# Performance work log

Hardware: AMD Instinct MI355X
Metric: run time of the kernel (lower is better)

## Reference

```python
import jax, jax.numpy as jnp
import numpy as np

HIDDEN = 1024

def setup_inputs() -> dict:
    key = jax.random.key(0)
    ks = jax.random.split(key, 7)
    s = 1.0 / np.sqrt(HIDDEN)
    X = jax.random.normal(ks[0], (4, 2048, HIDDEN), dtype=jnp.float32)
    Wq = jax.random.uniform(ks[1], (HIDDEN, HIDDEN), jnp.float32, -s, s)
    bq = jax.random.uniform(ks[2], (HIDDEN,), jnp.float32, -s, s)
    Wk = jax.random.uniform(ks[3], (HIDDEN, HIDDEN), jnp.float32, -s, s)
    bk = jax.random.uniform(ks[4], (HIDDEN,), jnp.float32, -s, s)
    Wv = jax.random.uniform(ks[5], (HIDDEN, HIDDEN), jnp.float32, -s, s)
    bv = jax.random.uniform(ks[6], (HIDDEN,), jnp.float32, -s, s)
    return {"X": X, "Wq": Wq, "bq": bq, "Wk": Wk, "bk": bk, "Wv": Wv, "bv": bv}

def reference(X, Wq, bq, Wk, bk, Wv, bv):
    # torch Linear: x @ W.T + b
    q = jnp.einsum('bsd,ed->bse', X, Wq) + bq  # [B,S,H]
    k = jnp.einsum('bsd,ed->bse', X, Wk) + bk
    v = jnp.einsum('bsd,ed->bse', X, Wv) + bv
    scores = jnp.einsum('bqd,bkd->bqk', q, k) / jnp.sqrt(jnp.float32(HIDDEN))  # [B,S,S]
    attn = jax.nn.softmax(scores, axis=-1)
    return jnp.einsum('bqk,bkd->bqd', attn, v)
```

## Files before the change

### kernel.cpp

```cpp
#include <hip/hip_runtime.h>
#include <hip/hip_bf16.h>
#include <stdint.h>

#define B_ 4
#define S_ 2048
#define H_ 1024

typedef __attribute__((ext_vector_type(4))) float f32x4;
typedef __attribute__((ext_vector_type(8))) short bf16x8;

#define AS1C(p) ((const __attribute__((address_space(1))) void*)(p))
#define AS3(p)  ((__attribute__((address_space(3))) void*)(p))

__global__ __launch_bounds__(256)
void f32_to_bf16_k(const float* __restrict__ in, __hip_bfloat16* __restrict__ out, int n4) {
    int i = blockIdx.x * blockDim.x + threadIdx.x;
    if (i < n4) {
        float4 v = ((const float4*)in)[i];
        union { __hip_bfloat16 h[4]; uint64_t u; } o;
        o.h[0] = __float2bfloat16(v.x);
        o.h[1] = __float2bfloat16(v.y);
        o.h[2] = __float2bfloat16(v.z);
        o.h[3] = __float2bfloat16(v.w);
        ((uint64_t*)out)[i] = o.u;
    }
}

__global__ __launch_bounds__(256)
void pack_bias_k(const float* __restrict__ b0, const float* __restrict__ b1,
                 const float* __restrict__ b2, float* __restrict__ out) {
    int i = blockIdx.x * blockDim.x + threadIdx.x;
    const float* src = (i < H_) ? b0 : (i < 2 * H_) ? b1 : b2;
    out[i] = src[i & (H_ - 1)];
}

template<bool OUT_BF16, bool HAS_BIAS>
__global__ __launch_bounds__(256)
void gemm_bt(const __hip_bfloat16* __restrict__ A, int lda, long long aBatch,
             const __hip_bfloat16* __restrict__ B, int ldb, long long bBatch,
             const float* __restrict__ bias,
             void* __restrict__ Cout, int ldc, long long cBatch,
             int M, int N, int K, float scale)
{
    __shared__ __hip_bfloat16 lA[128 * 64];
    __shared__ __hip_bfloat16 lB[128 * 64];

    const int t  = threadIdx.x;
    const int bz = blockIdx.z;
    A += (long long)bz * aBatch;
    B += (long long)bz * bBatch;
    const int bm = blockIdx.y * 128;
    const int bn = blockIdx.x * 128;

    const int wave = t >> 6;
    const int lane = t & 63;
    const int wm = (wave & 1) * 64;
    const int wn = (wave >> 1) * 64;
    const int lm = lane & 15;
    const int kq = lane >> 4;

    f32x4 acc[4][4] = {};

    const int srow = t >> 3;
    const int swz  = ((t & 7) ^ ((t >> 3) & 7)) * 8;
    const __hip_bfloat16* gA = A + (long long)(bm + srow) * lda + swz;
    const __hip_bfloat16* gB = B + (long long)(bn + srow) * ldb + swz;
    __hip_bfloat16* sA = lA + t * 8;
    __hip_bfloat16* sB = lB + t * 8;

    const int cro = lm & 7;

    for (int k0 = 0; k0 < K; k0 += 64) {
        __syncthreads();
#pragma unroll
        for (int s = 0; s < 4; ++s) {
            __builtin_amdgcn_global_load_lds(AS1C(gA + (long long)s * 32 * lda + k0),
                                             AS3(sA + s * 2048), 16, 0, 0);
            __builtin_amdgcn_global_load_lds(AS1C(gB + (long long)s * 32 * ldb + k0),
                                             AS3(sB + s * 2048), 16, 0, 0);
        }
        __syncthreads();

#pragma unroll
        for (int ks = 0; ks < 2; ++ks) {
            bf16x8 af[4], bfr[4];
            const int ch = ((ks * 4 + kq) ^ cro) * 8;
#pragma unroll
            for (int i = 0; i < 4; ++i) {
                af[i]  = *(const bf16x8*)(lA + (wm + i * 16 + lm) * 64 + ch);
                bfr[i] = *(const bf16x8*)(lB + (wn + i * 16 + lm) * 64 + ch);
            }
#pragma unroll
            for (int i = 0; i < 4; ++i)
#pragma unroll
                for (int j = 0; j < 4; ++j)
                    acc[i][j] = __builtin_amdgcn_mfma_f32_16x16x32_bf16(af[i], bfr[j], acc[i][j], 0, 0, 0);
        }
    }

    const int r0 = kq * 4;
#pragma unroll
    for (int j = 0; j < 4; ++j) {
        const int col = bn + wn + j * 16 + lm;
        float bvv = 0.0f;
        if (HAS_BIAS) bvv = bias[col];
#pragma unroll
        for (int i = 0; i < 4; ++i) {
            const int rowb = bm + wm + i * 16 + r0;
#pragma unroll
            for (int r = 0; r < 4; ++r) {
                float val = acc[i][j][r] * scale + bvv;
                long long idx = (long long)bz * cBatch + (long long)(rowb + r) * ldc + col;
                if (OUT_BF16) ((__hip_bfloat16*)Cout)[idx] = __float2bfloat16(val);
                else          ((float*)Cout)[idx] = val;
            }
        }
    }
}

__global__ __launch_bounds__(256)
void transpose64(const __hip_bfloat16* __restrict__ in, int ld_in, long long inBatch,
                 __hip_bfloat16* __restrict__ out, long long outBatch,
                 int rows, int cols)
{
    __shared__ __hip_bfloat16 tile[64][66];
    in  += (long long)blockIdx.z * inBatch;
    out += (long long)blockIdx.z * outBatch;
    const int c0 = blockIdx.x * 64;
    const int r0 = blockIdx.y * 64;
    const int tc  = threadIdx.x & 63;
    const int tr4 = threadIdx.x >> 6;
#pragma unroll
    for (int r = tr4; r < 64; r += 4)
        tile[r][tc] = in[(long long)(r0 + r) * ld_in + c0 + tc];
    __syncthreads();
#pragma unroll
    for (int r = tr4; r < 64; r += 4)
        out[(long long)(c0 + r) * rows + r0 + tc] = tile[tc][r];
}

__global__ __launch_bounds__(256)
void softmax_rows(__hip_bfloat16* __restrict__ s, int cols)
{
    __shared__ float red[4];
    __shared__ float red2[4];
    __hip_bfloat16* p = s + (long long)blockIdx.x * cols;
    const int t = threadIdx.x;

    union { uint4 u; __hip_bfloat16 h[8]; } in;
    in.u = *(const uint4*)(p + t * 8);
    float v[8];
    float mx = -1e30f;
#pragma unroll
    for (int i = 0; i < 8; ++i) {
        v[i] = __bfloat162float(in.h[i]);
        mx = fmaxf(mx, v[i]);
    }
#pragma unroll
    for (int off = 32; off; off >>= 1) mx = fmaxf(mx, __shfl_down(mx, off));
    if ((t & 63) == 0) red[t >> 6] = mx;
    __syncthreads();
    mx = fmaxf(fmaxf(red[0], red[1]), fmaxf(red[2], red[3]));

    float sum = 0.0f;
#pragma unroll
    for (int i = 0; i < 8; ++i) { v[i] = __expf(v[i] - mx); sum += v[i]; }
#pragma unroll
    for (int off = 32; off; off >>= 1) sum += __shfl_down(sum, off);
    if ((t & 63) == 0) red2[t >> 6] = sum;
    __syncthreads();
    sum = red2[0] + red2[1] + red2[2] + red2[3];
    float inv = 1.0f / sum;
    union { uint4 u; __hip_bfloat16 h[8]; } o;
#pragma unroll
    for (int i = 0; i < 8; ++i) o.h[i] = __float2bfloat16(v[i] * inv);
    *(uint4*)(p + t * 8) = o.u;
}

extern "C" void kernel_launch(void* const* d_in, const int* in_sizes, int n_in,
                              void* d_out, int out_size, void* d_ws, size_t ws_size,
                              hipStream_t stream)
{
    const float* X  = (const float*)d_in[0];
    const float* Wq = (const float*)d_in[1];
    const float* bq = (const float*)d_in[2];
    const float* Wk = (const float*)d_in[3];
    const float* bk = (const float*)d_in[4];
    const float* Wv = (const float*)d_in[5];
    const float* bv = (const float*)d_in[6];
    float* out = (float*)d_out;

    char* w = (char*)d_ws;
    const size_t MB = 1ull << 20;
    __hip_bfloat16* Xb   = (__hip_bfloat16*)(w + 0);
    __hip_bfloat16* Wall = (__hip_bfloat16*)(w + 16 * MB);
    float*          ball = (float*)        (w + 22 * MB);
    __hip_bfloat16* sc   = (__hip_bfloat16*)(w + 0);
    __hip_bfloat16* qkv  = (__hip_bfloat16*)(w + 32 * MB);
    __hip_bfloat16* vtb  = (__hip_bfloat16*)(w + 80 * MB);

    const int HH4 = H_ * H_ / 4;

    f32_to_bf16_k<<<(B_ * S_ * H_ / 4 + 255) / 256, 256, 0, stream>>>(X, Xb, B_ * S_ * H_ / 4);
    f32_to_bf16_k<<<(HH4 + 255) / 256, 256, 0, stream>>>(Wq, Wall, HH4);
    f32_to_bf16_k<<<(HH4 + 255) / 256, 256, 0, stream>>>(Wk, Wall + H_ * H_, HH4);
    f32_to_bf16_k<<<(HH4 + 255) / 256, 256, 0, stream>>>(Wv, Wall + 2 * H_ * H_, HH4);
    pack_bias_k<<<(3 * H_) / 256, 256, 0, stream>>>(bq, bk, bv, ball);

    dim3 g1(3 * H_ / 128, (B_ * S_) / 128, 1);
    gemm_bt<true, true><<<g1, 256, 0, stream>>>(
        Xb, H_, 0, Wall, H_, 0, ball, qkv, 3 * H_, 0, B_ * S_, 3 * H_, H_, 1.0f);

    transpose64<<<dim3(H_ / 64, S_ / 64, B_), 256, 0, stream>>>(
        qkv + 2 * H_, 3 * H_, (long long)S_ * 3 * H_, vtb, (long long)H_ * S_, S_, H_);

    dim3 g2(S_ / 128, S_ / 128, B_);
    gemm_bt<true, false><<<g2, 256, 0, stream>>>(
        qkv,      3 * H_, (long long)S_ * 3 * H_,
        qkv + H_, 3 * H_, (long long)S_ * 3 * H_,
        nullptr, sc, S_, (long long)S_ * S_, S_, S_, H_, 0.03125f);

    softmax_rows<<<B_ * S_, 256, 0, stream>>>(sc, S_);

    dim3 g3(H_ / 128, S_ / 128, B_);
    gemm_bt<false, false><<<g3, 256, 0, stream>>>(
        sc,  S_, (long long)S_ * S_,
        vtb, S_, (long long)H_ * S_,
        nullptr, out, H_, (long long)S_ * H_, S_, H_, S_, 1.0f);
}
```

Before: 271.3 us.

## Switch GEMM to 32x32x16 MFMA, fuse V transpose into QKV epilogue, merge weight converts

Moves the GEMM inner loop from 16x16x32 to 32x32x16 bf16 MFMA with a 2x2 accumulator tile per wave, which cuts LDS fragment loads per MFMA. The QKV projection epilogue now writes the V block directly transposed into the vtb buffer, so the separate transpose kernel and its extra read and write pass go away. The three weight conversion launches are merged into one kernel. The transposed V stores are 8-byte column-strided writes, which may coalesce less well than the old row stores.

```diff
diff --git a/kernel.cpp b/kernel.cpp
--- a/kernel.cpp
+++ b/kernel.cpp
@@ -6,7 +6,7 @@
 #define S_ 2048
 #define H_ 1024
 
-typedef __attribute__((ext_vector_type(4))) float f32x4;
+typedef __attribute__((ext_vector_type(16))) float f32x16;
 typedef __attribute__((ext_vector_type(8))) short bf16x8;
 
 #define AS1C(p) ((const __attribute__((address_space(1))) void*)(p))
@@ -27,6 +27,22 @@
 }
 
 __global__ __launch_bounds__(256)
+void conv_weights_k(const float* __restrict__ w0, const float* __restrict__ w1,
+                    const float* __restrict__ w2, __hip_bfloat16* __restrict__ out) {
+    const int per = H_ * H_ / 4;
+    int i = blockIdx.x * blockDim.x + threadIdx.x;
+    const float* src = (i < per) ? w0 : (i < 2 * per) ? w1 : w2;
+    int li = i - ((i < per) ? 0 : (i < 2 * per) ? per : 2 * per);
+    float4 v = ((const float4*)src)[li];
+    union { __hip_bfloat16 h[4]; uint64_t u; } o;
+    o.h[0] = __float2bfloat16(v.x);
+    o.h[1] = __float2bfloat16(v.y);
+    o.h[2] = __float2bfloat16(v.z);
+    o.h[3] = __float2bfloat16(v.w);
+    ((uint64_t*)out)[i] = o.u;
+}
+
+__global__ __launch_bounds__(256)
 void pack_bias_k(const float* __restrict__ b0, const float* __restrict__ b1,
                  const float* __restrict__ b2, float* __restrict__ out) {
     int i = blockIdx.x * blockDim.x + threadIdx.x;
@@ -34,12 +50,13 @@
     out[i] = src[i & (H_ - 1)];
 }
 
-template<bool OUT_BF16, bool HAS_BIAS>
+template<bool OUT_BF16, bool HAS_BIAS, bool V_SPLIT>
 __global__ __launch_bounds__(256)
 void gemm_bt(const __hip_bfloat16* __restrict__ A, int lda, long long aBatch,
              const __hip_bfloat16* __restrict__ B, int ldb, long long bBatch,
              const float* __restrict__ bias,
              void* __restrict__ Cout, int ldc, long long cBatch,
+             __hip_bfloat16* __restrict__ vtrans,
              int M, int N, int K, float scale)
 {
     __shared__ __hip_bfloat16 lA[128 * 64];
@@ -56,10 +73,10 @@
     const int lane = t & 63;
     const int wm = (wave & 1) * 64;
     const int wn = (wave >> 1) * 64;
-    const int lm = lane & 15;
-    const int kq = lane >> 4;
-
-    f32x4 acc[4][4] = {};
+    const int lr = lane & 31;
+    const int kh = lane >> 5;
+
+    f32x16 acc[2][2] = {};
 
     const int srow = t >> 3;
     const int swz  = ((t & 7) ^ ((t >> 3) & 7)) * 8;
@@ -67,8 +84,6 @@
     const __hip_bfloat16* gB = B + (long long)(bn + srow) * ldb + swz;
     __hip_bfloat16* sA = lA + t * 8;
     __hip_bfloat16* sB = lB + t * 8;
-
-    const int cro = lm & 7;
 
     for (int k0 = 0; k0 < K; k0 += 64) {
         __syncthreads();
@@ -82,61 +97,55 @@
         __syncthreads();
 
 #pragma unroll
-        for (int ks = 0; ks < 2; ++ks) {
-            bf16x8 af[4], bfr[4];
-            const int ch = ((ks * 4 + kq) ^ cro) * 8;
-#pragma unroll
-            for (int i = 0; i < 4; ++i) {
-                af[i]  = *(const bf16x8*)(lA + (wm + i * 16 + lm) * 64 + ch);
-                bfr[i] = *(const bf16x8*)(lB + (wn + i * 16 + lm) * 64 + ch);
+        for (int ks = 0; ks < 4; ++ks) {
+            bf16x8 af[2], bfr[2];
+            const int ch = ((ks * 2 + kh) ^ (lane & 7)) * 8;
+#pragma unroll
+            for (int i = 0; i < 2; ++i) {
+                af[i]  = *(const bf16x8*)(lA + (wm + i * 32 + lr) * 64 + ch);
+                bfr[i] = *(const bf16x8*)(lB + (wn + i * 32 + lr) * 64 + ch);
             }
 #pragma unroll
-            for (int i = 0; i < 4; ++i)
-#pragma unroll
-                for (int j = 0; j < 4; ++j)
-                    acc[i][j] = __builtin_amdgcn_mfma_f32_16x16x32_bf16(af[i], bfr[j], acc[i][j], 0, 0, 0);
+            for (int i = 0; i < 2; ++i)
+#pragma unroll
+                for (int j = 0; j < 2; ++j)
+                    acc[i][j] = __builtin_amdgcn_mfma_f32_32x32x16_bf16(af[i], bfr[j], acc[i][j], 0, 0, 0);
         }
     }
 
-    const int r0 = kq * 4;
-#pragma unroll
-    for (int j = 0; j < 4; ++j) {
-        const int col = bn + wn + j * 16 + lm;
+    const bool vmode = V_SPLIT && (bn >= 2 * H_);
+#pragma unroll
+    for (int j = 0; j < 2; ++j) {
+        const int col = bn + wn + j * 32 + lr;
         float bvv = 0.0f;
         if (HAS_BIAS) bvv = bias[col];
 #pragma unroll
-        for (int i = 0; i < 4; ++i) {
-            const int rowb = bm + wm + i * 16 + r0;
-#pragma unroll
-            for (int r = 0; r < 4; ++r) {
-                float val = acc[i][j][r] * scale + bvv;
-                long long idx = (long long)bz * cBatch + (long long)(rowb + r) * ldc + col;
-                if (OUT_BF16) ((__hip_bfloat16*)Cout)[idx] = __float2bfloat16(val);
-                else          ((float*)Cout)[idx] = val;
+        for (int i = 0; i < 2; ++i) {
+            const int rowb = bm + wm + i * 32 + 4 * kh;
+            if (!vmode) {
+#pragma unroll
+                for (int g = 0; g < 4; ++g)
+#pragma unroll
+                    for (int r = 0; r < 4; ++r) {
+                        float val = acc[i][j][g * 4 + r] * scale + bvv;
+                        long long idx = (long long)bz * cBatch + (long long)(rowb + g * 8 + r) * ldc + col;
+                        if (OUT_BF16) ((__hip_bfloat16*)Cout)[idx] = __float2bfloat16(val);
+                        else          ((float*)Cout)[idx] = val;
+                    }
+            } else {
+                const long long ebase = (long long)((rowb >> 11) * H_ + col - 2 * H_) * S_;
+                const int s0 = rowb & 2047;
+#pragma unroll
+                for (int g = 0; g < 4; ++g) {
+                    union { ushort4 u; __hip_bfloat16 h[4]; } o;
+#pragma unroll
+                    for (int r = 0; r < 4; ++r)
+                        o.h[r] = __float2bfloat16(acc[i][j][g * 4 + r] * scale + bvv);
+                    *(ushort4*)(vtrans + ebase + s0 + g * 8) = o.u;
+                }
             }
         }
     }
-}
-
-__global__ __launch_bounds__(256)
-void transpose64(const __hip_bfloat16* __restrict__ in, int ld_in, long long inBatch,
-                 __hip_bfloat16* __restrict__ out, long long outBatch,
-                 int rows, int cols)
-{
-    __shared__ __hip_bfloat16 tile[64][66];
-    in  += (long long)blockIdx.z * inBatch;
-    out += (long long)blockIdx.z * outBatch;
-    const int c0 = blockIdx.x * 64;
-    const int r0 = blockIdx.y * 64;
-    const int tc  = threadIdx.x & 63;
-    const int tr4 = threadIdx.x >> 6;
-#pragma unroll
-    for (int r = tr4; r < 64; r += 4)
-        tile[r][tc] = in[(long long)(r0 + r) * ld_in + c0 + tc];
-    __syncthreads();
-#pragma unroll
-    for (int r = tr4; r < 64; r += 4)
-        out[(long long)(c0 + r) * rows + r0 + tc] = tile[tc][r];
 }
 
 __global__ __launch_bounds__(256)
@@ -199,32 +208,25 @@
     __hip_bfloat16* qkv  = (__hip_bfloat16*)(w + 32 * MB);
     __hip_bfloat16* vtb  = (__hip_bfloat16*)(w + 80 * MB);
 
-    const int HH4 = H_ * H_ / 4;
-
     f32_to_bf16_k<<<(B_ * S_ * H_ / 4 + 255) / 256, 256, 0, stream>>>(X, Xb, B_ * S_ * H_ / 4);
-    f32_to_bf16_k<<<(HH4 + 255) / 256, 256, 0, stream>>>(Wq, Wall, HH4);
-    f32_to_bf16_k<<<(HH4 + 255) / 256, 256, 0, stream>>>(Wk, Wall + H_ * H_, HH4);
-    f32_to_bf16_k<<<(HH4 + 255) / 256, 256, 0, stream>>>(Wv, Wall + 2 * H_ * H_, HH4);
+    conv_weights_k<<<(3 * H_ * H_ / 4 + 255) / 256, 256, 0, stream>>>(Wq, Wk, Wv, Wall);
     pack_bias_k<<<(3 * H_) / 256, 256, 0, stream>>>(bq, bk, bv, ball);
 
     dim3 g1(3 * H_ / 128, (B_ * S_) / 128, 1);
-    gemm_bt<true, true><<<g1, 256, 0, stream>>>(
-        Xb, H_, 0, Wall, H_, 0, ball, qkv, 3 * H_, 0, B_ * S_, 3 * H_, H_, 1.0f);
-
-    transpose64<<<dim3(H_ / 64, S_ / 64, B_), 256, 0, stream>>>(
-        qkv + 2 * H_, 3 * H_, (long long)S_ * 3 * H_, vtb, (long long)H_ * S_, S_, H_);
+    gemm_bt<true, true, true><<<g1, 256, 0, stream>>>(
+        Xb, H_, 0, Wall, H_, 0, ball, qkv, 3 * H_, 0, vtb, B_ * S_, 3 * H_, H_, 1.0f);
 
     dim3 g2(S_ / 128, S_ / 128, B_);
-    gemm_bt<true, false><<<g2, 256, 0, stream>>>(
+    gemm_bt<true, false, false><<<g2, 256, 0, stream>>>(
         qkv,      3 * H_, (long long)S_ * 3 * H_,
         qkv + H_, 3 * H_, (long long)S_ * 3 * H_,
-        nullptr, sc, S_, (long long)S_ * S_, S_, S_, H_, 0.03125f);
+        nullptr, sc, S_, (long long)S_ * S_, nullptr, S_, S_, H_, 0.03125f);
 
     softmax_rows<<<B_ * S_, 256, 0, stream>>>(sc, S_);
 
     dim3 g3(H_ / 128, S_ / 128, B_);
-    gemm_bt<false, false><<<g3, 256, 0, stream>>>(
+    gemm_bt<false, false, false><<<g3, 256, 0, stream>>>(
         sc,  S_, (long long)S_ * S_,
         vtb, S_, (long long)H_ * S_,
-        nullptr, out, H_, (long long)S_ * H_, S_, H_, S_, 1.0f);
-}
+        nullptr, out, H_, (long long)S_ * H_, nullptr, S_, H_, S_, 1.0f);
+}
```

Result: no change. 268.2 us (-1.2%).

## Double-buffer GEMM LDS tiles, fuse V transpose into QKV epilogue, merge prep kernels

Applied to the files above, without the earlier changes.

The bf16 GEMM now keeps two LDS buffers and issues the next K-tile's global-to-LDS loads before computing on the current one, waiting with vmcnt so memory latency overlaps with MFMA work. The QKV projection writes its V columns straight into a transposed layout, which removes the separate transpose kernel and its extra pass over V. The four conversion kernels and the bias-pack kernel are merged into one launch. Doubling LDS to 64KB per block may lower occupancy, and the transposed V stores are narrower and strided.

```diff
diff --git a/kernel.cpp b/kernel.cpp
--- a/kernel.cpp
+++ b/kernel.cpp
@@ -13,37 +13,55 @@
 #define AS3(p)  ((__attribute__((address_space(3))) void*)(p))
 
 __global__ __launch_bounds__(256)
-void f32_to_bf16_k(const float* __restrict__ in, __hip_bfloat16* __restrict__ out, int n4) {
+void prep_k(const float* __restrict__ X,
+            const float* __restrict__ Wq, const float* __restrict__ Wk,
+            const float* __restrict__ Wv,
+            const float* __restrict__ bq, const float* __restrict__ bk,
+            const float* __restrict__ bv,
+            __hip_bfloat16* __restrict__ Xb, __hip_bfloat16* __restrict__ Wall,
+            float* __restrict__ ball)
+{
+    const int NX = B_ * S_ * H_ / 4;
+    const int NW = H_ * H_ / 4;
     int i = blockIdx.x * blockDim.x + threadIdx.x;
-    if (i < n4) {
-        float4 v = ((const float4*)in)[i];
+    if (i < NX + 3 * NW) {
+        const float* src; uint64_t* dst; int li;
+        if (i < NX) { src = X; dst = (uint64_t*)Xb; li = i; }
+        else {
+            int j = i - NX;
+            int wsel = j / NW; li = j - wsel * NW;
+            src = (wsel == 0) ? Wq : (wsel == 1) ? Wk : Wv;
+            dst = (uint64_t*)Wall + (size_t)wsel * NW;
+        }
+        float4 v = ((const float4*)src)[li];
         union { __hip_bfloat16 h[4]; uint64_t u; } o;
         o.h[0] = __float2bfloat16(v.x);
         o.h[1] = __float2bfloat16(v.y);
         o.h[2] = __float2bfloat16(v.z);
         o.h[3] = __float2bfloat16(v.w);
-        ((uint64_t*)out)[i] = o.u;
-    }
-}
-
-__global__ __launch_bounds__(256)
-void pack_bias_k(const float* __restrict__ b0, const float* __restrict__ b1,
-                 const float* __restrict__ b2, float* __restrict__ out) {
-    int i = blockIdx.x * blockDim.x + threadIdx.x;
-    const float* src = (i < H_) ? b0 : (i < 2 * H_) ? b1 : b2;
-    out[i] = src[i & (H_ - 1)];
-}
-
-template<bool OUT_BF16, bool HAS_BIAS>
+        dst[li] = o.u;
+    } else {
+        int j = i - (NX + 3 * NW);
+        if (j < 3 * H_ / 4) {
+            int bsel = j >> 8;
+            int off  = j & 255;
+            const float* src = (bsel == 0) ? bq : (bsel == 1) ? bk : bv;
+            ((float4*)ball)[j] = ((const float4*)src)[off];
+        }
+    }
+}
+
+template<bool OUT_BF16, bool HAS_BIAS, bool V_SPLIT>
 __global__ __launch_bounds__(256)
 void gemm_bt(const __hip_bfloat16* __restrict__ A, int lda, long long aBatch,
              const __hip_bfloat16* __restrict__ B, int ldb, long long bBatch,
              const float* __restrict__ bias,
              void* __restrict__ Cout, int ldc, long long cBatch,
+             __hip_bfloat16* __restrict__ vtrans,
              int M, int N, int K, float scale)
 {
-    __shared__ __hip_bfloat16 lA[128 * 64];
-    __shared__ __hip_bfloat16 lB[128 * 64];
+    __shared__ __hip_bfloat16 lA[2][128 * 64];
+    __shared__ __hip_bfloat16 lB[2][128 * 64];
 
     const int t  = threadIdx.x;
     const int bz = blockIdx.z;
@@ -58,6 +76,7 @@
     const int wn = (wave >> 1) * 64;
     const int lm = lane & 15;
     const int kq = lane >> 4;
+    const int cro = lm & 7;
 
     f32x4 acc[4][4] = {};
 
@@ -65,21 +84,32 @@
     const int swz  = ((t & 7) ^ ((t >> 3) & 7)) * 8;
     const __hip_bfloat16* gA = A + (long long)(bm + srow) * lda + swz;
     const __hip_bfloat16* gB = B + (long long)(bn + srow) * ldb + swz;
-    __hip_bfloat16* sA = lA + t * 8;
-    __hip_bfloat16* sB = lB + t * 8;
-
-    const int cro = lm & 7;
-
-    for (int k0 = 0; k0 < K; k0 += 64) {
-        __syncthreads();
-#pragma unroll
-        for (int s = 0; s < 4; ++s) {
-            __builtin_amdgcn_global_load_lds(AS1C(gA + (long long)s * 32 * lda + k0),
-                                             AS3(sA + s * 2048), 16, 0, 0);
-            __builtin_amdgcn_global_load_lds(AS1C(gB + (long long)s * 32 * ldb + k0),
-                                             AS3(sB + s * 2048), 16, 0, 0);
-        }
-        __syncthreads();
+
+    const int NIT = K >> 6;
+
+#define STAGE(buf, kk)                                                              \
+    {                                                                               \
+        __hip_bfloat16* sA = &lA[buf][0] + t * 8;                                   \
+        __hip_bfloat16* sB = &lB[buf][0] + t * 8;                                   \
+        _Pragma("unroll")                                                           \
+        for (int s = 0; s < 4; ++s) {                                               \
+            __builtin_amdgcn_global_load_lds(AS1C(gA + (long long)s * 32 * lda + (kk)), \
+                                             AS3(sA + s * 2048), 16, 0, 0);         \
+            __builtin_amdgcn_global_load_lds(AS1C(gB + (long long)s * 32 * ldb + (kk)), \
+                                             AS3(sB + s * 2048), 16, 0, 0);         \
+        }                                                                           \
+    }
+
+    STAGE(0, 0);
+
+    for (int it = 0; it < NIT; ++it) {
+        const int cur = it & 1;
+        if (it + 1 < NIT) {
+            STAGE(cur ^ 1, (it + 1) << 6);
+            asm volatile("s_waitcnt vmcnt(8)\n\ts_barrier" ::: "memory");
+        } else {
+            asm volatile("s_waitcnt vmcnt(0)\n\ts_barrier" ::: "memory");
+        }
 
 #pragma unroll
         for (int ks = 0; ks < 2; ++ks) {
@@ -87,8 +117,8 @@
             const int ch = ((ks * 4 + kq) ^ cro) * 8;
 #pragma unroll
             for (int i = 0; i < 4; ++i) {
-                af[i]  = *(const bf16x8*)(lA + (wm + i * 16 + lm) * 64 + ch);
-                bfr[i] = *(const bf16x8*)(lB + (wn + i * 16 + lm) * 64 + ch);
+                af[i]  = *(const bf16x8*)(&lA[cur][0] + (wm + i * 16 + lm) * 64 + ch);
+                bfr[i] = *(const bf16x8*)(&lB[cur][0] + (wn + i * 16 + lm) * 64 + ch);
             }
 #pragma unroll
             for (int i = 0; i < 4; ++i)
@@ -96,9 +126,14 @@
                 for (int j = 0; j < 4; ++j)
                     acc[i][j] = __builtin_amdgcn_mfma_f32_16x16x32_bf16(af[i], bfr[j], acc[i][j], 0, 0, 0);
         }
-    }
-
-    const int r0 = kq * 4;
+
+        if (it + 1 < NIT)
+            asm volatile("s_barrier" ::: "memory");
+    }
+#undef STAGE
+
+    const bool vmode = V_SPLIT && (bn >= 2 * H_);
+    const int r0q = kq * 4;
 #pragma unroll
     for (int j = 0; j < 4; ++j) {
         const int col = bn + wn + j * 16 + lm;
@@ -106,37 +141,25 @@
         if (HAS_BIAS) bvv = bias[col];
 #pragma unroll
         for (int i = 0; i < 4; ++i) {
-            const int rowb = bm + wm + i * 16 + r0;
-#pragma unroll
-            for (int r = 0; r < 4; ++r) {
-                float val = acc[i][j][r] * scale + bvv;
-                long long idx = (long long)bz * cBatch + (long long)(rowb + r) * ldc + col;
-                if (OUT_BF16) ((__hip_bfloat16*)Cout)[idx] = __float2bfloat16(val);
-                else          ((float*)Cout)[idx] = val;
+            const int rowb = bm + wm + i * 16 + r0q;
+            if (!vmode) {
+#pragma unroll
+                for (int r = 0; r < 4; ++r) {
+                    float val = acc[i][j][r] * scale + bvv;
+                    long long idx = (long long)bz * cBatch + (long long)(rowb + r) * ldc + col;
+                    if (OUT_BF16) ((__hip_bfloat16*)Cout)[idx] = __float2bfloat16(val);
+                    else          ((float*)Cout)[idx] = val;
+                }
+            } else {
+                const long long ebase = (long long)((rowb >> 11) * H_ + col - 2 * H_) * S_;
+                union { ushort4 u; __hip_bfloat16 h[4]; } o;
+#pragma unroll
+                for (int r = 0; r < 4; ++r)
+                    o.h[r] = __float2bfloat16(acc[i][j][r] * scale + bvv);
+                *(ushort4*)(vtrans + ebase + (rowb & 2047)) = o.u;
             }
         }
     }
-}
-
-__global__ __launch_bounds__(256)
-void transpose64(const __hip_bfloat16* __restrict__ in, int ld_in, long long inBatch,
-                 __hip_bfloat16* __restrict__ out, long long outBatch,
-                 int rows, int cols)
-{
-    __shared__ __hip_bfloat16 tile[64][66];
-    in  += (long long)blockIdx.z * inBatch;
-    out += (long long)blockIdx.z * outBatch;
-    const int c0 = blockIdx.x * 64;
-    const int r0 = blockIdx.y * 64;
-    const int tc  = threadIdx.x & 63;
-    const int tr4 = threadIdx.x >> 6;
-#pragma unroll
-    for (int r = tr4; r < 64; r += 4)
-        tile[r][tc] = in[(long long)(r0 + r) * ld_in + c0 + tc];
-    __syncthreads();
-#pragma unroll
-    for (int r = tr4; r < 64; r += 4)
-        out[(long long)(c0 + r) * rows + r0 + tc] = tile[tc][r];
 }
 
 __global__ __launch_bounds__(256)
@@ -199,32 +222,25 @@
     __hip_bfloat16* qkv  = (__hip_bfloat16*)(w + 32 * MB);
     __hip_bfloat16* vtb  = (__hip_bfloat16*)(w + 80 * MB);
 
-    const int HH4 = H_ * H_ / 4;
-
-    f32_to_bf16_k<<<(B_ * S_ * H_ / 4 + 255) / 256, 256, 0, stream>>>(X, Xb, B_ * S_ * H_ / 4);
-    f32_to_bf16_k<<<(HH4 + 255) / 256, 256, 0, stream>>>(Wq, Wall, HH4);
-    f32_to_bf16_k<<<(HH4 + 255) / 256, 256, 0, stream>>>(Wk, Wall + H_ * H_, HH4);
-    f32_to_bf16_k<<<(HH4 + 255) / 256, 256, 0, stream>>>(Wv, Wall + 2 * H_ * H_, HH4);
-    pack_bias_k<<<(3 * H_) / 256, 256, 0, stream>>>(bq, bk, bv, ball);
+    const int prep_items = B_ * S_ * H_ / 4 + 3 * H_ * H_ / 4 + 3 * H_ / 4;
+    prep_k<<<(prep_items + 255) / 256, 256, 0, stream>>>(X, Wq, Wk, Wv, bq, bk, bv,
+                                                         Xb, Wall, ball);
 
     dim3 g1(3 * H_ / 128, (B_ * S_) / 128, 1);
-    gemm_bt<true, true><<<g1, 256, 0, stream>>>(
-        Xb, H_, 0, Wall, H_, 0, ball, qkv, 3 * H_, 0, B_ * S_, 3 * H_, H_, 1.0f);
-
-    transpose64<<<dim3(H_ / 64, S_ / 64, B_), 256, 0, stream>>>(
-        qkv + 2 * H_, 3 * H_, (long long)S_ * 3 * H_, vtb, (long long)H_ * S_, S_, H_);
+    gemm_bt<true, true, true><<<g1, 256, 0, stream>>>(
+        Xb, H_, 0, Wall, H_, 0, ball, qkv, 3 * H_, 0, vtb, B_ * S_, 3 * H_, H_, 1.0f);
 
     dim3 g2(S_ / 128, S_ / 128, B_);
-    gemm_bt<true, false><<<g2, 256, 0, stream>>>(
+    gemm_bt<true, false, false><<<g2, 256, 0, stream>>>(
         qkv,      3 * H_, (long long)S_ * 3 * H_,
         qkv + H_, 3 * H_, (long long)S_ * 3 * H_,
-        nullptr, sc, S_, (long long)S_ * S_, S_, S_, H_, 0.03125f);
+        nullptr, sc, S_, (long long)S_ * S_, nullptr, S_, S_, H_, 0.03125f);
 
     softmax_rows<<<B_ * S_, 256, 0, stream>>>(sc, S_);
 
     dim3 g3(H_ / 128, S_ / 128, B_);
-    gemm_bt<false, false><<<g3, 256, 0, stream>>>(
+    gemm_bt<false, false, false><<<g3, 256, 0, stream>>>(
         sc,  S_, (long long)S_ * S_,
         vtb, S_, (long long)H_ * S_,
-        nullptr, out, H_, (long long)S_ * H_, S_, H_, S_, 1.0f);
-}
+        nullptr, out, H_, (long long)S_ * H_, nullptr, S_, H_, S_, 1.0f);
+}
```

Result: faster. 263.7 us (-2.8%).
